# Kernel optimization log

Measured on AMD Instinct MI355X. Metric: run time of the kernel, lower is better.

## Reference

```python
import jax, jax.numpy as jnp
import numpy as np

EPS = 1e-6

def setup_inputs() -> dict:
    key = jax.random.key(0)
    kq, kk, kv = jax.random.split(key, 3)
    n, L, h, d = 4, 8192, 8, 64
    queries = jax.random.normal(kq, (n, L, h, d), dtype=jnp.float32)
    keys = jax.random.normal(kk, (n, L, h, d), dtype=jnp.float32)
    values = jax.random.normal(kv, (n, L, h, d), dtype=jnp.float32)
    return {"queries": queries, "keys": keys, "values": values}

def reference(queries, keys, values):
    d = queries.shape[-1]
    temp = d ** (-0.25)  # softmax_temp default e**-0.25
    # elu feature map: phi(x) = elu(x) + 1  (applied after temperature scaling)
    q = jax.nn.elu(queries * temp) + 1.0  # [n, l, h, d]
    k = jax.nn.elu(keys * temp) + 1.0     # [n, s, h, d]
    # associative kv state: [n, h, m, d]
    kv = jnp.einsum('nshd,nshm->nhmd', k, values)
    # normalizer z: [n, l, h]
    z = 1.0 / (jnp.einsum('nlhd,nhd->nlh', q, k.sum(axis=1)) + EPS)
    # output: [n, l, h, m]
    v = jnp.einsum('nlhd,nhmd,nlh->nlhm', q, kv, z)
    # module returns v.transpose(-3, -2) -> [n, h, l, m]
    return jnp.swapaxes(v, 1, 2)
```

## Files before the change

kernel.cpp:

```cpp
#include <hip/hip_runtime.h>
#include <hip/hip_bf16.h>

#define NN 4
#define LL 8192
#define HH 8
#define DD 64
#define NH 32
#define RS  (HH*DD)
#define KV_ELEMS 4160
#define CCH 128

typedef __attribute__((ext_vector_type(8))) short bf16x8;
typedef __attribute__((ext_vector_type(4))) float f32x4;

__device__ __forceinline__ float phi(float x) {
  float t = x * 0.35355339059327373f;
  return t > 0.f ? t + 1.f : __expf(t);
}
__device__ __forceinline__ short f2bf(float x) {
  __hip_bfloat16 h = __float2bfloat16(x);
  return (short)__builtin_bit_cast(unsigned short, h);
}
__device__ __forceinline__ float bf2f(short s) {
  __hip_bfloat16 h = __builtin_bit_cast(__hip_bfloat16, (unsigned short)s);
  return __bfloat162float(h);
}
__device__ __forceinline__ void split2(float x, short& hi, short& lo) {
  hi = f2bf(x);
  lo = f2bf(x - bf2f(hi));
}
#define MFMA16 __builtin_amdgcn_mfma_f32_16x16x32_bf16

__global__ __launch_bounds__(512, 1) void kv_partial_kernel(
    const float* __restrict__ K, const float* __restrict__ V,
    float* __restrict__ part, int sch)
{
  const int n = blockIdx.x / sch, chunk = blockIdx.x % sch;
  const int tid = threadIdx.x;
  const int w = tid >> 6, lane = tid & 63;
  const int q = lane >> 4, p = lane & 15;
  const int cq = tid >> 7;
  const int cg = tid & 127;
  const int rows_pb = LL / sch;
  const int nsteps = rows_pb / 32;

  const float* kbase = K + ((size_t)n * LL + (size_t)chunk * rows_pb) * RS;
  const float* vbase = V + ((size_t)n * LL + (size_t)chunk * rows_pb) * RS;

  __shared__ short pl[4][512 * 32];

  f32x4 acc[4][4] = {};
  float ksacc[4] = {0.f, 0.f, 0.f, 0.f};
  f32x4 kr[8], vr[8];

  auto loadregs = [&](int T) {
    const float* kp = kbase + (size_t)(T * 32 + cq * 8) * RS + 4 * cg;
    const float* vp = vbase + (size_t)(T * 32 + cq * 8) * RS + 4 * cg;
#pragma unroll
    for (int u = 0; u < 8; ++u) {
      kr[u] = *(const f32x4*)(kp + (size_t)u * RS);
      vr[u] = *(const f32x4*)(vp + (size_t)u * RS);
    }
  };
  auto cw = [&]() {
#pragma unroll
    for (int j = 0; j < 4; ++j) {
      const int col = 4 * cg + j;
      const int pos = (cq ^ ((col ^ (col >> 2)) & 3)) * 8;
      bf16x8 kh, kl, vh, vl;
      float s = 0.f;
#pragma unroll
      for (int u = 0; u < 8; ++u) {
        float f = phi(kr[u][j]);
        s += f;
        short a, b;
        split2(f, a, b);          kh[u] = a; kl[u] = b;
        split2(vr[u][j], a, b);   vh[u] = a; vl[u] = b;
      }
      ksacc[j] += s;
      *(bf16x8*)&pl[0][col * 32 + pos] = kh;
      *(bf16x8*)&pl[1][col * 32 + pos] = kl;
      *(bf16x8*)&pl[2][col * 32 + pos] = vh;
      *(bf16x8*)&pl[3][col * 32 + pos] = vl;
    }
  };

  loadregs(0);
  for (int t = 0; t < nsteps; ++t) {
    cw();
    __syncthreads();
    if (t + 1 < nsteps) loadregs(t + 1);

    bf16x8 ah[4], al[4], bh[4], bl[4];
#pragma unroll
    for (int dt = 0; dt < 4; ++dt) {
      const int col = w * 64 + dt * 16 + p;
      const int pos = (q ^ ((col ^ (col >> 2)) & 3)) * 8;
      ah[dt] = *(const bf16x8*)&pl[0][col * 32 + pos];
      al[dt] = *(const bf16x8*)&pl[1][col * 32 + pos];
      bh[dt] = *(const bf16x8*)&pl[2][col * 32 + pos];
      bl[dt] = *(const bf16x8*)&pl[3][col * 32 + pos];
    }
#pragma unroll
    for (int dt = 0; dt < 4; ++dt)
#pragma unroll
      for (int mt = 0; mt < 4; ++mt) {
        acc[dt][mt] = MFMA16(ah[dt], bh[mt], acc[dt][mt], 0, 0, 0);
        acc[dt][mt] = MFMA16(ah[dt], bl[mt], acc[dt][mt], 0, 0, 0);
        acc[dt][mt] = MFMA16(al[dt], bh[mt], acc[dt][mt], 0, 0, 0);
      }
    __syncthreads();
  }

  float* po = part + ((size_t)blockIdx.x * 8 + w) * KV_ELEMS;
#pragma unroll
  for (int dt = 0; dt < 4; ++dt)
#pragma unroll
    for (int mt = 0; mt < 4; ++mt)
#pragma unroll
      for (int r = 0; r < 4; ++r)
        po[(dt * 16 + q * 4 + r) * 64 + mt * 16 + p] = acc[dt][mt][r];

  float* ksl = (float*)pl;
  f32x4 kq = {ksacc[0], ksacc[1], ksacc[2], ksacc[3]};
  *(f32x4*)&ksl[cq * 520 + 4 * cg] = kq;
  __syncthreads();
  {
    float s = ksl[tid] + ksl[520 + tid] + ksl[1040 + tid] + ksl[1560 + tid];
    part[((size_t)blockIdx.x * 8 + (tid >> 6)) * KV_ELEMS + 4096 + (tid & 63)] = s;
  }
}

__global__ __launch_bounds__(256) void kv_reduce_kernel(
    const float* __restrict__ part, short* __restrict__ kvh,
    short* __restrict__ kvl, float* __restrict__ ksum, int np)
{
  const int nh = blockIdx.x / 17;
  const int e  = (blockIdx.x % 17) * 256 + threadIdx.x;
  if (e >= KV_ELEMS) return;
  const int n = nh >> 3, hh = nh & 7;
  const float* pp = part + ((size_t)(n * np) * 8 + hh) * KV_ELEMS + e;
  float s = 0.f;
  for (int i = 0; i < np; ++i) s += pp[(size_t)i * 8 * KV_ELEMS];
  if (e < 4096) {
    const int d = e >> 6, m = e & 63;
    short hi, lo; split2(s, hi, lo);
    kvh[(size_t)nh * 4096 + m * 64 + d] = hi;
    kvl[(size_t)nh * 4096 + m * 64 + d] = lo;
  } else {
    ksum[(size_t)nh * 64 + (e - 4096)] = s;
  }
}

__global__ __launch_bounds__(512, 2) void attn_out_kernel(
    const float* __restrict__ Q, const short* __restrict__ kvh,
    const short* __restrict__ kvl, const float* __restrict__ ksumg,
    float* __restrict__ out)
{
  const int n = blockIdx.x / CCH, chunk = blockIdx.x % CCH;
  const int tid = threadIdx.x;
  const int w = tid >> 6, lane = tid & 63;
  const int q = lane >> 4, p = lane & 15;
  const int nh = n * 8 + w;
  const int rows_pb = LL / CCH;
  const int nt = rows_pb / 16;
  const int l_base = chunk * rows_pb;
  const int sr = tid >> 5, sc = (tid & 31) * 16;

  const float* qbase = Q + (size_t)n * LL * RS;

  __shared__ short qh[16][520];
  __shared__ short ql[16][520];

  bf16x8 bh[4][2], bl[4][2];
#pragma unroll
  for (int mt = 0; mt < 4; ++mt)
#pragma unroll
    for (int kst = 0; kst < 2; ++kst) {
      const size_t off = (size_t)nh * 4096 + (size_t)(mt * 16 + p) * 64 + kst * 32 + q * 8;
      bh[mt][kst] = *(const bf16x8*)(kvh + off);
      bl[mt][kst] = *(const bf16x8*)(kvl + off);
    }
  float ksr[2][8];
#pragma unroll
  for (int kst = 0; kst < 2; ++kst) {
    const float* kp = ksumg + (size_t)nh * 64 + kst * 32 + q * 8;
    f32x4 a = *(const f32x4*)(kp), b = *(const f32x4*)(kp + 4);
    ksr[kst][0]=a[0]; ksr[kst][1]=a[1]; ksr[kst][2]=a[2]; ksr[kst][3]=a[3];
    ksr[kst][4]=b[0]; ksr[kst][5]=b[1]; ksr[kst][6]=b[2]; ksr[kst][7]=b[3];
  }

  f32x4 qa[4], qb[4];
  auto loadq = [&](f32x4* R, int T) {
    const float* qp_ = qbase + (size_t)(l_base + T * 16 + sr) * RS + sc;
    R[0] = *(const f32x4*)(qp_);      R[1] = *(const f32x4*)(qp_ + 4);
    R[2] = *(const f32x4*)(qp_ + 8);  R[3] = *(const f32x4*)(qp_ + 12);
  };

  auto cbody = [&](const f32x4* R, int T) {
    bf16x8 hv0, hv1, lv0, lv1;
#pragma unroll
    for (int r = 0; r < 2; ++r)
#pragma unroll
      for (int jj = 0; jj < 4; ++jj) {
        float f = phi(R[r][jj]);
        short hs, ls; split2(f, hs, ls);
        hv0[r * 4 + jj] = hs; lv0[r * 4 + jj] = ls;
      }
#pragma unroll
    for (int r = 0; r < 2; ++r)
#pragma unroll
      for (int jj = 0; jj < 4; ++jj) {
        float f = phi(R[r + 2][jj]);
        short hs, ls; split2(f, hs, ls);
        hv1[r * 4 + jj] = hs; lv1[r * 4 + jj] = ls;
      }
    *(bf16x8*)&qh[sr][sc]     = hv0;  *(bf16x8*)&qh[sr][sc + 8] = hv1;
    *(bf16x8*)&ql[sr][sc]     = lv0;  *(bf16x8*)&ql[sr][sc + 8] = lv1;
    __syncthreads();

    f32x4 acc[4] = {};
    float zp = 0.f;
    bf16x8 ah[2], al[2];
#pragma unroll
    for (int kst = 0; kst < 2; ++kst) {
      const int cc = w * 64 + kst * 32 + q * 8;
      ah[kst] = *(const bf16x8*)&qh[p][cc];
      al[kst] = *(const bf16x8*)&ql[p][cc];
#pragma unroll
      for (int j = 0; j < 8; ++j)
        zp += (bf2f(ah[kst][j]) + bf2f(al[kst][j])) * ksr[kst][j];
    }
    __syncthreads();

#pragma unroll
    for (int kst = 0; kst < 2; ++kst)
#pragma unroll
      for (int mt = 0; mt < 4; ++mt) {
        acc[mt] = MFMA16(ah[kst], bh[mt][kst], acc[mt], 0, 0, 0);
        acc[mt] = MFMA16(ah[kst], bl[mt][kst], acc[mt], 0, 0, 0);
        acc[mt] = MFMA16(al[kst], bh[mt][kst], acc[mt], 0, 0, 0);
      }
    zp += __shfl_xor(zp, 16, 64);
    zp += __shfl_xor(zp, 32, 64);
    const float z = 1.0f / (zp + 1e-6f);
    float zr[4];
#pragma unroll
    for (int r = 0; r < 4; ++r) zr[r] = __shfl(z, q * 4 + r, 64);

    const int l0 = l_base + T * 16;
#pragma unroll
    for (int mt = 0; mt < 4; ++mt)
#pragma unroll
      for (int r = 0; r < 4; ++r)
        out[((size_t)nh * LL + l0 + q * 4 + r) * DD + mt * 16 + p] = acc[mt][r] * zr[r];
  };

  loadq(qa, 0);
  for (int t = 0; t < nt; t += 2) {
    loadq(qb, t + 1);
    cbody(qa, t);
    if (t + 2 < nt) loadq(qa, t + 2);
    cbody(qb, t + 1);
  }
}

extern "C" void kernel_launch(void* const* d_in, const int* in_sizes, int n_in,
                              void* d_out, int out_size, void* d_ws, size_t ws_size,
                              hipStream_t stream)
{
  const float* Q = (const float*)d_in[0];
  const float* K = (const float*)d_in[1];
  const float* V = (const float*)d_in[2];
  float* out = (float*)d_out;

  int sch = 64;
  while (sch > 4) {
    size_t need = (size_t)NN * sch * 8 * KV_ELEMS * 4
                + (size_t)NH * 4096 * 2 * 2
                + (size_t)NH * 64 * 4;
    if (need <= ws_size) break;
    sch >>= 1;
  }
  float* part = (float*)d_ws;
  short* kvh  = (short*)((char*)d_ws + (size_t)NN * sch * 8 * KV_ELEMS * 4);
  short* kvl  = kvh + (size_t)NH * 4096;
  float* ksum = (float*)(kvl + (size_t)NH * 4096);

  hipLaunchKernelGGL(kv_partial_kernel, dim3(NN * sch), dim3(512), 0, stream,
                     K, V, part, sch);
  hipLaunchKernelGGL(kv_reduce_kernel, dim3(NH * 17), dim3(256), 0, stream,
                     part, kvh, kvl, ksum, sch);
  hipLaunchKernelGGL(attn_out_kernel, dim3(NN * CCH), dim3(512), 0, stream,
                     Q, kvh, kvl, ksum, out);
}
```

Baseline: 245.7 us.

## Double-buffer K/V register prefetch and use barriers that skip vmcnt waits

The kv_partial loop now holds two register sets of K/V tiles and prefetches two steps ahead, so global loads have a full extra iteration to land. __syncthreads is replaced by a custom barrier that waits only on LDS counters (lgkmcnt), not on outstanding vector memory loads. This lets prefetches stay in flight across barriers. The cost is doubled register use for the staging buffers, which may cause spills at 512 threads. The loop also assumes nsteps is even.

Result: slower. 272.6 us (+10.9%).

```diff
diff --git a/kernel.cpp b/kernel.cpp
--- a/kernel.cpp
+++ b/kernel.cpp
@@ -30,6 +30,13 @@
   lo = f2bf(x - bf2f(hi));
 }
 #define MFMA16 __builtin_amdgcn_mfma_f32_16x16x32_bf16
+
+#define BARRIER_NOVM() do {                                   \
+    asm volatile("s_waitcnt lgkmcnt(0)" ::: "memory");        \
+    __builtin_amdgcn_sched_barrier(0);                        \
+    __builtin_amdgcn_s_barrier();                             \
+    __builtin_amdgcn_sched_barrier(0);                        \
+  } while (0)
 
 __global__ __launch_bounds__(512, 1) void kv_partial_kernel(
     const float* __restrict__ K, const float* __restrict__ V,
@@ -51,9 +58,9 @@
 
   f32x4 acc[4][4] = {};
   float ksacc[4] = {0.f, 0.f, 0.f, 0.f};
-  f32x4 kr[8], vr[8];
-
-  auto loadregs = [&](int T) {
+  f32x4 krA[8], vrA[8], krB[8], vrB[8];
+
+  auto loadregs = [&](int T, f32x4 (&kr)[8], f32x4 (&vr)[8]) {
     const float* kp = kbase + (size_t)(T * 32 + cq * 8) * RS + 4 * cg;
     const float* vp = vbase + (size_t)(T * 32 + cq * 8) * RS + 4 * cg;
 #pragma unroll
@@ -62,7 +69,7 @@
       vr[u] = *(const f32x4*)(vp + (size_t)u * RS);
     }
   };
-  auto cw = [&]() {
+  auto cw = [&](f32x4 (&kr)[8], f32x4 (&vr)[8]) {
 #pragma unroll
     for (int j = 0; j < 4; ++j) {
       const int col = 4 * cg + j;
@@ -84,13 +91,7 @@
       *(bf16x8*)&pl[3][col * 32 + pos] = vl;
     }
   };
-
-  loadregs(0);
-  for (int t = 0; t < nsteps; ++t) {
-    cw();
-    __syncthreads();
-    if (t + 1 < nsteps) loadregs(t + 1);
-
+  auto mfma_step = [&]() {
     bf16x8 ah[4], al[4], bh[4], bl[4];
 #pragma unroll
     for (int dt = 0; dt < 4; ++dt) {
@@ -109,7 +110,22 @@
         acc[dt][mt] = MFMA16(ah[dt], bl[mt], acc[dt][mt], 0, 0, 0);
         acc[dt][mt] = MFMA16(al[dt], bh[mt], acc[dt][mt], 0, 0, 0);
       }
-    __syncthreads();
+  };
+
+  loadregs(0, krA, vrA);
+  loadregs(1, krB, vrB);
+  for (int t = 0; t < nsteps; t += 2) {
+    cw(krA, vrA);
+    BARRIER_NOVM();
+    if (t + 2 < nsteps) loadregs(t + 2, krA, vrA);
+    mfma_step();
+    BARRIER_NOVM();
+
+    cw(krB, vrB);
+    BARRIER_NOVM();
+    if (t + 3 < nsteps) loadregs(t + 3, krB, vrB);
+    mfma_step();
+    BARRIER_NOVM();
   }
 
   float* po = part + ((size_t)blockIdx.x * 8 + w) * KV_ELEMS;
@@ -217,7 +233,7 @@
       }
     *(bf16x8*)&qh[sr][sc]     = hv0;  *(bf16x8*)&qh[sr][sc + 8] = hv1;
     *(bf16x8*)&ql[sr][sc]     = lv0;  *(bf16x8*)&ql[sr][sc + 8] = lv1;
-    __syncthreads();
+    BARRIER_NOVM();
 
     f32x4 acc[4] = {};
     float zp = 0.f;
@@ -231,7 +247,7 @@
       for (int j = 0; j < 8; ++j)
         zp += (bf2f(ah[kst][j]) + bf2f(al[kst][j])) * ksr[kst][j];
     }
-    __syncthreads();
+    BARRIER_NOVM();
 
 #pragma unroll
     for (int kst = 0; kst < 2; ++kst)
```
